# Kernel tuning notes

Measured on AMD Instinct MI355X. Metric: run time of the kernel, lower is better.

The kernel has to match this reference:

```python
import jax, jax.numpy as jnp
import numpy as np

INPUT_DIM = 6
HIDDEN = 256
NUM_CLASSES = 8
B = 16
V = 32768


def setup_inputs() -> dict:
    key = jax.random.key(0)
    ks = jax.random.split(key, 8)
    x = jax.random.normal(ks[0], (B, INPUT_DIM, V), dtype=jnp.float32)
    obj_idx = jax.random.randint(ks[1], (B,), 0, NUM_CLASSES)
    # Stacked per-class expert weights (Conv1d kernel_size=1 == pointwise linear)
    s1 = 1.0 / np.sqrt(INPUT_DIM)
    s2 = 1.0 / np.sqrt(HIDDEN)
    w1 = jax.random.uniform(ks[2], (NUM_CLASSES, HIDDEN, INPUT_DIM), jnp.float32, -s1, s1)
    b1 = jax.random.uniform(ks[3], (NUM_CLASSES, HIDDEN), jnp.float32, -s1, s1)
    w2 = jax.random.uniform(ks[4], (NUM_CLASSES, HIDDEN, HIDDEN), jnp.float32, -s2, s2)
    b2 = jax.random.uniform(ks[5], (NUM_CLASSES, HIDDEN), jnp.float32, -s2, s2)
    w3 = jax.random.uniform(ks[6], (NUM_CLASSES, 1, HIDDEN), jnp.float32, -s2, s2)
    b3 = jax.random.uniform(ks[7], (NUM_CLASSES, 1), jnp.float32, -s2, s2)
    return {"x": x, "obj_idx": obj_idx, "w1": w1, "b1": b1,
            "w2": w2, "b2": b2, "w3": w3, "b3": b3}


def reference(x, obj_idx, w1, b1, w2, b2, w3, b3):
    # Gather each sample's expert weights, then run the fused 3-layer pointwise
    # MLP over all B*V positions in one batched einsum per layer (no Python
    # loop over samples, unlike the original torch code).
    # x: [B, 6, V] -> out: [B, 1, V]
    h = jax.nn.relu(jnp.einsum('boi,biv->bov', w1[obj_idx], x) + b1[obj_idx][:, :, None])
    h = jax.nn.relu(jnp.einsum('boi,biv->bov', w2[obj_idx], h) + b2[obj_idx][:, :, None])
    out = jnp.einsum('boi,biv->bov', w3[obj_idx], h) + b3[obj_idx][:, :, None]
    return out
```

## Files before the change

### kernel.cpp

```cpp
#include <hip/hip_runtime.h>
#include <hip/hip_bf16.h>

typedef __bf16 bf16x8 __attribute__((ext_vector_type(8)));
typedef __bf16 bf16x4 __attribute__((ext_vector_type(4)));
typedef float  f32x4  __attribute__((ext_vector_type(4)));
typedef float  f32x16 __attribute__((ext_vector_type(16)));

#define V_TOTAL 32768
#define NT      512
#define NV      32
#define NBLK    256

#define W2_LDS  32768
#define H1_LDS  32768
#define RED_LDS 2048
#define LDS_TOT (W2_LDS + H1_LDS + RED_LDS)

#define GLOAD_LDS16(g, l) __builtin_amdgcn_global_load_lds( \
    (const __attribute__((address_space(1))) void*)(g),     \
    (__attribute__((address_space(3))) void*)(l), 16, 0, 0)

__global__ void w2_to_bf16(const float* __restrict__ w2, __bf16* __restrict__ w2b) {
    int i = blockIdx.x * 256 + threadIdx.x;
    int e = i >> 16, q = i & 65535;
    int c = q >> 9, w = q & 511, lane = w >> 3, j = w & 7;
    int ks = c >> 3, tile = c & 7;
    int m = tile * 32 + (lane & 31);
    int k = ks * 16 + (lane >> 5) * 8 + j;
    w2b[i] = (__bf16)w2[e * 65536 + m * 256 + k];
}

__global__ __launch_bounds__(NT) void fused_mlp(
    const float* __restrict__ x,  const int* __restrict__ obj,
    const float* __restrict__ w1, const float* __restrict__ b1,
    const float* __restrict__ b2, const float* __restrict__ w3,
    const float* __restrict__ b3, const __bf16* __restrict__ w2b,
    float* __restrict__ out)
{
    extern __shared__ __align__(16) char smem[];
    char*  w2s = smem;
    char*  h1t = smem + W2_LDS;
    float* red = (float*)(smem + W2_LDS + H1_LDS);

    const int t    = threadIdx.x;
    const int lane = t & 63;
    const int wv   = t >> 6;
    const int c32  = lane & 31;
    const int hh   = lane >> 5;
    const int b    = blockIdx.x >> 4;
    const int g    = blockIdx.x & 15;
    const int e    = __builtin_amdgcn_readfirstlane(obj[b]);
    const __bf16* w2sw = w2b + (size_t)e * 65536;

    #pragma unroll
    for (int it = 0; it < 4; ++it) {
        int c0 = it * 8 + wv;
        GLOAD_LDS16(w2sw + c0 * 512 + lane * 8, w2s + c0 * 1024);
    }

    bf16x8 aar[12];
    #pragma unroll
    for (int k2 = 0; k2 < 12; ++k2)
        aar[k2] = *(const bf16x8*)(w2sw + ((4 + k2) * 8 + wv) * 512 + lane * 8);

    const float* w1e = w1 + e * 1536;
    const float* b1e = b1 + e * 256;
    const float* b2e = b2 + e * 256;
    const float* w3e = w3 + e * 256;
    bf16x8 aa1 = {};
    if (hh == 0)
        #pragma unroll
        for (int j = 0; j < 6; ++j) aa1[j] = (__bf16)w1e[(wv * 32 + c32) * 6 + j];
    const float b3e = b3[e];
    const float* xe = x + (size_t)b * 6 * V_TOTAL;

    bf16x8 xf[2];
    auto load_x = [&](int ic) {
        #pragma unroll
        for (int pt = 0; pt < 2; ++pt) {
            bf16x8 v = {};
            #pragma unroll
            for (int i = 0; i < 6; ++i)
                v[i] = (__bf16)xe[i * V_TOTAL + (g * NV + ic) * 64 + pt * 32 + c32];
            xf[pt] = v;
        }
    };
    auto do_l1 = [&]() {
        f32x16 b1f;
        #pragma unroll
        for (int gg = 0; gg < 4; ++gg) {
            f32x4 v = *(const f32x4*)(b1e + wv * 32 + gg * 8 + hh * 4);
            #pragma unroll
            for (int q = 0; q < 4; ++q) b1f[gg * 4 + q] = v[q];
        }
        #pragma unroll
        for (int pt = 0; pt < 2; ++pt) {
            f32x16 h = __builtin_amdgcn_mfma_f32_32x32x16_bf16(aa1, xf[pt], b1f, 0, 0, 0);
            #pragma unroll
            for (int gg = 0; gg < 4; ++gg) {
                bf16x4 pk;
                #pragma unroll
                for (int q = 0; q < 4; ++q) pk[q] = (__bf16)fmaxf(h[gg * 4 + q], 0.f);
                *(bf16x4*)(h1t + ((wv * 2 + (gg >> 1)) * 2 + pt) * 1024
                           + (gg & 1) * 512 + c32 * 16 + hh * 8) = pk;
            }
        }
    };

    load_x(0);

    for (int iv = 0; iv < NV; ++iv) {
        do_l1();
        if (iv + 1 < NV) load_x(iv + 1);
        __syncthreads();

        f32x16 acc0, acc1;
        #pragma unroll
        for (int gg = 0; gg < 4; ++gg) {
            f32x4 v = *(const f32x4*)(b2e + wv * 32 + gg * 8 + hh * 4);
            #pragma unroll
            for (int q = 0; q < 4; ++q) { acc0[gg * 4 + q] = v[q]; acc1[gg * 4 + q] = v[q]; }
        }
        const char* bbase = h1t + lane * 16;
        #pragma unroll
        for (int ks = 0; ks < 4; ++ks) {
            const bf16x8 aw = *(const bf16x8*)(w2s + (ks * 8 + wv) * 1024 + lane * 16);
            const bf16x8 bb0 = *(const bf16x8*)(bbase + (ks * 2 + 0) * 1024);
            const bf16x8 bb1 = *(const bf16x8*)(bbase + (ks * 2 + 1) * 1024);
            acc0 = __builtin_amdgcn_mfma_f32_32x32x16_bf16(aw, bb0, acc0, 0, 0, 0);
            acc1 = __builtin_amdgcn_mfma_f32_32x32x16_bf16(aw, bb1, acc1, 0, 0, 0);
        }
        #pragma unroll
        for (int k2 = 0; k2 < 12; ++k2) {
            const bf16x8 bb0 = *(const bf16x8*)(bbase + ((4 + k2) * 2 + 0) * 1024);
            const bf16x8 bb1 = *(const bf16x8*)(bbase + ((4 + k2) * 2 + 1) * 1024);
            acc0 = __builtin_amdgcn_mfma_f32_32x32x16_bf16(aar[k2], bb0, acc0, 0, 0, 0);
            acc1 = __builtin_amdgcn_mfma_f32_32x32x16_bf16(aar[k2], bb1, acc1, 0, 0, 0);
        }

        float p0 = 0.f, p1 = 0.f;
        #pragma unroll
        for (int gg = 0; gg < 4; ++gg) {
            f32x4 wq = *(const f32x4*)(w3e + wv * 32 + gg * 8 + hh * 4);
            #pragma unroll
            for (int q = 0; q < 4; ++q) {
                p0 = fmaf(wq[q], fmaxf(acc0[gg * 4 + q], 0.f), p0);
                p1 = fmaf(wq[q], fmaxf(acc1[gg * 4 + q], 0.f), p1);
            }
        }
        p0 += __shfl_xor(p0, 32, 64);
        p1 += __shfl_xor(p1, 32, 64);
        if (lane < 32) {
            red[wv * 64 + c32]      = p0;
            red[wv * 64 + 32 + c32] = p1;
        }
        __syncthreads();

        if (t < 64) {
            float s = b3e;
            #pragma unroll
            for (int w8 = 0; w8 < 8; ++w8) s += red[w8 * 64 + t];
            out[(size_t)b * V_TOTAL + (g * NV + iv) * 64 + t] = s;
        }
    }
}

extern "C" void kernel_launch(void* const* d_in, const int* in_sizes, int n_in,
                              void* d_out, int out_size, void* d_ws, size_t ws_size,
                              hipStream_t stream) {
    const float* x   = (const float*)d_in[0];
    const int*   obj = (const int*)d_in[1];
    const float* w1  = (const float*)d_in[2];
    const float* b1  = (const float*)d_in[3];
    const float* w2  = (const float*)d_in[4];
    const float* b2  = (const float*)d_in[5];
    const float* w3  = (const float*)d_in[6];
    const float* b3  = (const float*)d_in[7];
    float*  out = (float*)d_out;
    __bf16* w2b = (__bf16*)d_ws;

    (void)hipFuncSetAttribute((const void*)fused_mlp,
                              hipFuncAttributeMaxDynamicSharedMemorySize, LDS_TOT);

    w2_to_bf16<<<2048, 256, 0, stream>>>(w2, w2b);
    fused_mlp<<<NBLK, NT, LDS_TOT, stream>>>(x, obj, w1, b1, b2, w3, b3, w2b, out);
}
```

Measured before the change: 75.20 us.

## Double block size to two wave-groups sharing LDS W2, halving per-group iterations

Each block now runs 1024 threads as two groups of eight waves that work on alternating 64-column chunks, each with its own H1 tile and reduction buffer. The W2 slice in LDS is shared by both groups, and the loop count per group is halved. The aim is more waves per CU to hide MFMA and LDS latency and to amortize the W2 preload. In exchange LDS use grows to about 100KB per block, and the block-wide barriers now couple the two groups.

```diff
diff --git a/kernel.cpp b/kernel.cpp
--- a/kernel.cpp
+++ b/kernel.cpp
@@ -7,13 +7,13 @@
 typedef float  f32x16 __attribute__((ext_vector_type(16)));
 
 #define V_TOTAL 32768
-#define NT      512
-#define NV      32
+#define NT      1024
+#define NVG     16
 #define NBLK    256
 
 #define W2_LDS  32768
-#define H1_LDS  32768
-#define RED_LDS 2048
+#define H1_LDS  65536
+#define RED_LDS 4096
 #define LDS_TOT (W2_LDS + H1_LDS + RED_LDS)
 
 #define GLOAD_LDS16(g, l) __builtin_amdgcn_global_load_lds( \
@@ -45,6 +45,8 @@
     const int t    = threadIdx.x;
     const int lane = t & 63;
     const int wv   = t >> 6;
+    const int gg2  = wv >> 3;
+    const int wvg  = wv & 7;
     const int c32  = lane & 31;
     const int hh   = lane >> 5;
     const int b    = blockIdx.x >> 4;
@@ -52,16 +54,19 @@
     const int e    = __builtin_amdgcn_readfirstlane(obj[b]);
     const __bf16* w2sw = w2b + (size_t)e * 65536;
 
+    char*  h1g  = h1t + gg2 * 32768;
+    float* redg = red + gg2 * 512;
+
     #pragma unroll
-    for (int it = 0; it < 4; ++it) {
-        int c0 = it * 8 + wv;
+    for (int it = 0; it < 2; ++it) {
+        int c0 = it * 16 + wv;
         GLOAD_LDS16(w2sw + c0 * 512 + lane * 8, w2s + c0 * 1024);
     }
 
     bf16x8 aar[12];
     #pragma unroll
     for (int k2 = 0; k2 < 12; ++k2)
-        aar[k2] = *(const bf16x8*)(w2sw + ((4 + k2) * 8 + wv) * 512 + lane * 8);
+        aar[k2] = *(const bf16x8*)(w2sw + ((4 + k2) * 8 + wvg) * 512 + lane * 8);
 
     const float* w1e = w1 + e * 1536;
     const float* b1e = b1 + e * 256;
@@ -70,18 +75,18 @@
     bf16x8 aa1 = {};
     if (hh == 0)
         #pragma unroll
-        for (int j = 0; j < 6; ++j) aa1[j] = (__bf16)w1e[(wv * 32 + c32) * 6 + j];
+        for (int j = 0; j < 6; ++j) aa1[j] = (__bf16)w1e[(wvg * 32 + c32) * 6 + j];
     const float b3e = b3[e];
     const float* xe = x + (size_t)b * 6 * V_TOTAL;
 
     bf16x8 xf[2];
-    auto load_x = [&](int ic) {
+    auto load_x = [&](int icb) {
         #pragma unroll
         for (int pt = 0; pt < 2; ++pt) {
             bf16x8 v = {};
             #pragma unroll
             for (int i = 0; i < 6; ++i)
-                v[i] = (__bf16)xe[i * V_TOTAL + (g * NV + ic) * 64 + pt * 32 + c32];
+                v[i] = (__bf16)xe[i * V_TOTAL + (g * 32 + icb) * 64 + pt * 32 + c32];
             xf[pt] = v;
         }
     };
@@ -89,7 +94,7 @@
         f32x16 b1f;
         #pragma unroll
         for (int gg = 0; gg < 4; ++gg) {
-            f32x4 v = *(const f32x4*)(b1e + wv * 32 + gg * 8 + hh * 4);
+            f32x4 v = *(const f32x4*)(b1e + wvg * 32 + gg * 8 + hh * 4);
             #pragma unroll
             for (int q = 0; q < 4; ++q) b1f[gg * 4 + q] = v[q];
         }
@@ -101,30 +106,32 @@
                 bf16x4 pk;
                 #pragma unroll
                 for (int q = 0; q < 4; ++q) pk[q] = (__bf16)fmaxf(h[gg * 4 + q], 0.f);
-                *(bf16x4*)(h1t + ((wv * 2 + (gg >> 1)) * 2 + pt) * 1024
+                *(bf16x4*)(h1g + ((wvg * 2 + (gg >> 1)) * 2 + pt) * 1024
                            + (gg & 1) * 512 + c32 * 16 + hh * 8) = pk;
             }
         }
     };
 
-    load_x(0);
+    load_x(gg2);
 
-    for (int iv = 0; iv < NV; ++iv) {
+    for (int iv = 0; iv < NVG; ++iv) {
+        const int icb = iv * 2 + gg2;
+
         do_l1();
-        if (iv + 1 < NV) load_x(iv + 1);
+        if (iv + 1 < NVG) load_x((iv + 1) * 2 + gg2);
         __syncthreads();
 
         f32x16 acc0, acc1;
         #pragma unroll
         for (int gg = 0; gg < 4; ++gg) {
-            f32x4 v = *(const f32x4*)(b2e + wv * 32 + gg * 8 + hh * 4);
+            f32x4 v = *(const f32x4*)(b2e + wvg * 32 + gg * 8 + hh * 4);
             #pragma unroll
             for (int q = 0; q < 4; ++q) { acc0[gg * 4 + q] = v[q]; acc1[gg * 4 + q] = v[q]; }
         }
-        const char* bbase = h1t + lane * 16;
+        const char* bbase = h1g + lane * 16;
         #pragma unroll
         for (int ks = 0; ks < 4; ++ks) {
-            const bf16x8 aw = *(const bf16x8*)(w2s + (ks * 8 + wv) * 1024 + lane * 16);
+            const bf16x8 aw = *(const bf16x8*)(w2s + (ks * 8 + wvg) * 1024 + lane * 16);
             const bf16x8 bb0 = *(const bf16x8*)(bbase + (ks * 2 + 0) * 1024);
             const bf16x8 bb1 = *(const bf16x8*)(bbase + (ks * 2 + 1) * 1024);
             acc0 = __builtin_amdgcn_mfma_f32_32x32x16_bf16(aw, bb0, acc0, 0, 0, 0);
@@ -141,7 +148,7 @@
         float p0 = 0.f, p1 = 0.f;
         #pragma unroll
         for (int gg = 0; gg < 4; ++gg) {
-            f32x4 wq = *(const f32x4*)(w3e + wv * 32 + gg * 8 + hh * 4);
+            f32x4 wq = *(const f32x4*)(w3e + wvg * 32 + gg * 8 + hh * 4);
             #pragma unroll
             for (int q = 0; q < 4; ++q) {
                 p0 = fmaf(wq[q], fmaxf(acc0[gg * 4 + q], 0.f), p0);
@@ -151,16 +158,16 @@
         p0 += __shfl_xor(p0, 32, 64);
         p1 += __shfl_xor(p1, 32, 64);
         if (lane < 32) {
-            red[wv * 64 + c32]      = p0;
-            red[wv * 64 + 32 + c32] = p1;
+            redg[wvg * 64 + c32]      = p0;
+            redg[wvg * 64 + 32 + c32] = p1;
         }
         __syncthreads();
 
-        if (t < 64) {
+        if (wvg == 0) {
             float s = b3e;
             #pragma unroll
-            for (int w8 = 0; w8 < 8; ++w8) s += red[w8 * 64 + t];
-            out[(size_t)b * V_TOTAL + (g * NV + iv) * 64 + t] = s;
+            for (int w8 = 0; w8 < 8; ++w8) s += redg[w8 * 64 + lane];
+            out[(size_t)b * V_TOTAL + (g * 32 + icb) * 64 + lane] = s;
         }
     }
 }
```

Result: slower. 138.7 us (+84.5%).
